# Kernel optimization log

Hardware: AMD Instinct MI355X
Metric: run time of the kernel (lower is better)

Reference implementation:

```python
import jax, jax.numpy as jnp
import numpy as np

N_NODES = 100000
N_EDGES = 1600000
D_FEAT = 128


def setup_inputs() -> dict:
    key = jax.random.key(0)
    k1, k2 = jax.random.split(key)
    x = jax.random.normal(k1, (N_NODES, D_FEAT), dtype=jnp.float32)
    edge_index = jax.random.randint(k2, (2, N_EDGES), 0, N_NODES, dtype=jnp.int64)
    return {"x": x, "edge_index": edge_index}


def reference(x, edge_index):
    # gather source/target node features: [E, D] each
    src = x[edge_index[0]]
    dst = x[edge_index[1]]
    # per-edge dot product -> [E], then sigmoid
    dot = jnp.sum(src * dst, axis=-1)
    return jax.nn.sigmoid(dot)
```

## Files before the change

kernel.cpp:

```cpp
#include <hip/hip_runtime.h>
#include <hip/hip_fp16.h>
#include <math.h>

#define D_FEAT 128

typedef _Float16 f16x2 __attribute__((ext_vector_type(2)));
struct alignas(16) h8v { f16x2 h[4]; };

__device__ __forceinline__ float dot8(const h8v& a, const h8v& b, float acc) {
#if __has_builtin(__builtin_amdgcn_fdot2)
#pragma unroll
    for (int k = 0; k < 4; ++k)
        acc = __builtin_amdgcn_fdot2(a.h[k], b.h[k], acc, false);
#else
#pragma unroll
    for (int k = 0; k < 4; ++k) {
        acc += (float)a.h[k].x * (float)b.h[k].x;
        acc += (float)a.h[k].y * (float)b.h[k].y;
    }
#endif
    return acc;
}

__device__ __forceinline__ float sigmoid_fast(float x) {
    return 1.0f / (1.0f + __builtin_exp2f(-1.44269504f * x));
}

__global__ __launch_bounds__(256) void convert_x_fp16_kernel(
    const float* __restrict__ x, __half* __restrict__ xh, int n_elems)
{
    int i = blockIdx.x * blockDim.x + threadIdx.x;
    int base = i * 8;
    if (base >= n_elems) return;
    const float4* p = reinterpret_cast<const float4*>(x + base);
    float4 f0 = p[0];
    float4 f1 = p[1];
    __half2 h[4];
    h[0] = __floats2half2_rn(f0.x, f0.y);
    h[1] = __floats2half2_rn(f0.z, f0.w);
    h[2] = __floats2half2_rn(f1.x, f1.y);
    h[3] = __floats2half2_rn(f1.z, f1.w);
    *reinterpret_cast<float4*>(xh + base) = *reinterpret_cast<float4*>(h);
}

__global__ __launch_bounds__(256) void edge_dot_sigmoid_fp16_kernel(
    const __half* __restrict__ xh,
    const int* __restrict__ ei,
    float* __restrict__ out,
    int n_edges)
{
    const int lane = threadIdx.x & 15;
    const int grp  = threadIdx.x >> 4;
    const int base = blockIdx.x * 32;
    const int e0 = base + grp;
    const int e1 = base + 16 + grp;

    if (e0 >= n_edges) return;

    const int s0 = ei[e0];
    const int d0 = ei[n_edges + e0];
    const bool has1 = (e1 < n_edges);
    const int s1 = has1 ? ei[e1] : s0;
    const int d1 = has1 ? ei[n_edges + e1] : d0;

    const h8v* __restrict__ xrow = reinterpret_cast<const h8v*>(xh);

    h8v a0 = xrow[(size_t)s0 * 16 + lane];
    h8v b0 = xrow[(size_t)d0 * 16 + lane];
    h8v a1 = xrow[(size_t)s1 * 16 + lane];
    h8v b1 = xrow[(size_t)d1 * 16 + lane];

    float acc0 = dot8(a0, b0, 0.f);
    float acc1 = dot8(a1, b1, 0.f);

    acc0 += __shfl_xor(acc0, 1, 16);
    acc0 += __shfl_xor(acc0, 2, 16);
    acc0 += __shfl_xor(acc0, 4, 16);
    acc0 += __shfl_xor(acc0, 8, 16);

    acc1 += __shfl_xor(acc1, 1, 16);
    acc1 += __shfl_xor(acc1, 2, 16);
    acc1 += __shfl_xor(acc1, 4, 16);
    acc1 += __shfl_xor(acc1, 8, 16);

    if (lane == 0) {
        out[e0] = sigmoid_fast(acc0);
        if (has1) out[e1] = sigmoid_fast(acc1);
    }
}

__global__ __launch_bounds__(256) void edge_dot_sigmoid_fp32_kernel(
    const float* __restrict__ x,
    const int* __restrict__ ei,
    float* __restrict__ out,
    int n_edges)
{
    const int lane = threadIdx.x & 15;
    const int e = blockIdx.x * 16 + (threadIdx.x >> 4);
    if (e >= n_edges) return;

    const int s = ei[e];
    const int d = ei[n_edges + e];

    const float4* sp = reinterpret_cast<const float4*>(x + (size_t)s * D_FEAT) + lane * 2;
    const float4* dp = reinterpret_cast<const float4*>(x + (size_t)d * D_FEAT) + lane * 2;

    float4 a0 = sp[0], a1 = sp[1], b0 = dp[0], b1 = dp[1];

    float acc = a0.x * b0.x + a0.y * b0.y + a0.z * b0.z + a0.w * b0.w
              + a1.x * b1.x + a1.y * b1.y + a1.z * b1.z + a1.w * b1.w;

    acc += __shfl_xor(acc, 1, 16);
    acc += __shfl_xor(acc, 2, 16);
    acc += __shfl_xor(acc, 4, 16);
    acc += __shfl_xor(acc, 8, 16);

    if (lane == 0) out[e] = sigmoid_fast(acc);
}

extern "C" void kernel_launch(void* const* d_in, const int* in_sizes, int n_in,
                              void* d_out, int out_size, void* d_ws, size_t ws_size,
                              hipStream_t stream) {
    const float* x   = (const float*)d_in[0];
    const int*   ei  = (const int*)d_in[1];
    float*       out = (float*)d_out;

    const int n_x     = in_sizes[0];
    const int n_edges = in_sizes[1] / 2;

    const size_t need = (size_t)n_x * sizeof(__half);
    if (ws_size >= need) {
        __half* xh = (__half*)d_ws;
        int n_chunks = (n_x + 7) / 8;
        convert_x_fp16_kernel<<<(n_chunks + 255) / 256, 256, 0, stream>>>(x, xh, n_x);
        dim3 grid((n_edges + 31) / 32);
        edge_dot_sigmoid_fp16_kernel<<<grid, 256, 0, stream>>>(xh, ei, out, n_edges);
    } else {
        dim3 grid((n_edges + 15) / 16);
        edge_dot_sigmoid_fp32_kernel<<<grid, 256, 0, stream>>>(x, ei, out, n_edges);
    }
}
```

Before: 111.5 us.

## Bucket edges by source node and swizzle workgroups across XCDs for cache locality

Adds a histogram, scan and scatter pipeline that bins edges by source node range into 1024 buckets. The dot kernel then walks the sorted edges, with workgroup ids remapped so each XCD handles a contiguous range, aiming for source row reuse in each XCD's L2. The cost is several extra kernel launches, atomics, extra index traffic (ss/sd/se arrays), and scattered output writes through the permutation.

```diff
diff --git a/kernel.cpp b/kernel.cpp
--- a/kernel.cpp
+++ b/kernel.cpp
@@ -3,6 +3,8 @@
 #include <math.h>
 
 #define D_FEAT 128
+#define NB 1024
+#define SCH 16384
 
 typedef _Float16 f16x2 __attribute__((ext_vector_type(2)));
 struct alignas(16) h8v { f16x2 h[4]; };
@@ -43,6 +45,122 @@
     *reinterpret_cast<float4*>(xh + base) = *reinterpret_cast<float4*>(h);
 }
 
+__global__ __launch_bounds__(256) void hist_kernel(
+    const int* __restrict__ ei, int n_edges, int shift, int* __restrict__ hist)
+{
+    __shared__ int h[NB];
+    for (int i = threadIdx.x; i < NB; i += 256) h[i] = 0;
+    __syncthreads();
+    for (int e = blockIdx.x * 256 + threadIdx.x; e < n_edges; e += gridDim.x * 256)
+        atomicAdd(&h[ei[e] >> shift], 1);
+    __syncthreads();
+    for (int i = threadIdx.x; i < NB; i += 256) {
+        int c = h[i];
+        if (c) atomicAdd(&hist[i], c);
+    }
+}
+
+__global__ __launch_bounds__(1024) void scan_kernel(
+    const int* __restrict__ hist, int* __restrict__ cursor)
+{
+    __shared__ int tmp[NB];
+    int t = threadIdx.x;
+    int own = hist[t];
+    tmp[t] = own;
+    __syncthreads();
+    for (int off = 1; off < NB; off <<= 1) {
+        int v = (t >= off) ? tmp[t - off] : 0;
+        __syncthreads();
+        tmp[t] += v;
+        __syncthreads();
+    }
+    cursor[t] = tmp[t] - own;
+}
+
+__global__ __launch_bounds__(256) void scatter_kernel(
+    const int* __restrict__ ei, int n_edges, int shift, int* __restrict__ cursor,
+    int* __restrict__ ss, int* __restrict__ sd, int* __restrict__ se)
+{
+    __shared__ int h[NB];
+    __shared__ int gbase[NB];
+    const int t = threadIdx.x;
+    for (int i = t; i < NB; i += 256) h[i] = 0;
+    __syncthreads();
+    const int c0 = blockIdx.x * SCH;
+    const int cend = min(n_edges, c0 + SCH);
+    for (int e = c0 + t; e < cend; e += 256)
+        atomicAdd(&h[ei[e] >> shift], 1);
+    __syncthreads();
+    for (int i = t; i < NB; i += 256) {
+        int c = h[i];
+        gbase[i] = c ? atomicAdd(&cursor[i], c) : 0;
+        h[i] = 0;
+    }
+    __syncthreads();
+    for (int e = c0 + t; e < cend; e += 256) {
+        int s = ei[e];
+        int b = s >> shift;
+        int loc = atomicAdd(&h[b], 1);
+        int pos = gbase[b] + loc;
+        ss[pos] = s;
+        sd[pos] = ei[n_edges + e];
+        se[pos] = e;
+    }
+}
+
+__global__ __launch_bounds__(256) void edge_dot_sigmoid_sorted_kernel(
+    const __half* __restrict__ xh,
+    const int* __restrict__ ss,
+    const int* __restrict__ sd,
+    const int* __restrict__ se,
+    float* __restrict__ out,
+    int n_edges, int q, int r)
+{
+    const int bid = blockIdx.x;
+    const int xcd = bid & 7;
+    const int idx = bid >> 3;
+    const int swz = (xcd < r) ? (xcd * (q + 1) + idx)
+                              : (r * (q + 1) + (xcd - r) * q + idx);
+
+    const int lane = threadIdx.x & 15;
+    const int grp  = threadIdx.x >> 4;
+    const int base = swz * 32;
+    const int e0 = base + grp;
+    const int e1 = base + 16 + grp;
+    if (e0 >= n_edges) return;
+
+    const int s0 = ss[e0];
+    const int d0 = sd[e0];
+    const bool has1 = (e1 < n_edges);
+    const int s1 = has1 ? ss[e1] : s0;
+    const int d1 = has1 ? sd[e1] : d0;
+
+    const h8v* __restrict__ xrow = reinterpret_cast<const h8v*>(xh);
+
+    h8v a0 = xrow[(size_t)s0 * 16 + lane];
+    h8v b0 = xrow[(size_t)d0 * 16 + lane];
+    h8v a1 = xrow[(size_t)s1 * 16 + lane];
+    h8v b1 = xrow[(size_t)d1 * 16 + lane];
+
+    float acc0 = dot8(a0, b0, 0.f);
+    float acc1 = dot8(a1, b1, 0.f);
+
+    acc0 += __shfl_xor(acc0, 1, 16);
+    acc0 += __shfl_xor(acc0, 2, 16);
+    acc0 += __shfl_xor(acc0, 4, 16);
+    acc0 += __shfl_xor(acc0, 8, 16);
+
+    acc1 += __shfl_xor(acc1, 1, 16);
+    acc1 += __shfl_xor(acc1, 2, 16);
+    acc1 += __shfl_xor(acc1, 4, 16);
+    acc1 += __shfl_xor(acc1, 8, 16);
+
+    if (lane == 0) {
+        out[se[e0]] = sigmoid_fast(acc0);
+        if (has1) out[se[e1]] = sigmoid_fast(acc1);
+    }
+}
+
 __global__ __launch_bounds__(256) void edge_dot_sigmoid_fp16_kernel(
     const __half* __restrict__ xh,
     const int* __restrict__ ei,
@@ -54,7 +172,6 @@
     const int base = blockIdx.x * 32;
     const int e0 = base + grp;
     const int e1 = base + 16 + grp;
-
     if (e0 >= n_edges) return;
 
     const int s0 = ei[e0];
@@ -127,9 +244,42 @@
 
     const int n_x     = in_sizes[0];
     const int n_edges = in_sizes[1] / 2;
-
-    const size_t need = (size_t)n_x * sizeof(__half);
-    if (ws_size >= need) {
+    const int n_nodes = n_x / D_FEAT;
+
+    size_t off_xh = 0;
+    size_t off_ss = ((size_t)n_x * 2 + 255) & ~(size_t)255;
+    size_t off_sd = off_ss + (size_t)n_edges * 4;
+    size_t off_se = off_sd + (size_t)n_edges * 4;
+    size_t off_hist = off_se + (size_t)n_edges * 4;
+    size_t off_cur  = off_hist + NB * 4;
+    size_t need_full = off_cur + NB * 4;
+    size_t need_fp16 = (size_t)n_x * 2;
+
+    if (ws_size >= need_full) {
+        __half* xh  = (__half*)((char*)d_ws + off_xh);
+        int* ss     = (int*)((char*)d_ws + off_ss);
+        int* sd     = (int*)((char*)d_ws + off_sd);
+        int* se     = (int*)((char*)d_ws + off_se);
+        int* hist   = (int*)((char*)d_ws + off_hist);
+        int* cursor = (int*)((char*)d_ws + off_cur);
+
+        int shift = 0;
+        while (((n_nodes - 1) >> shift) >= NB) shift++;
+
+        int n_chunks = (n_x + 7) / 8;
+        convert_x_fp16_kernel<<<(n_chunks + 255) / 256, 256, 0, stream>>>(x, xh, n_x);
+
+        hipMemsetAsync(hist, 0, NB * 4, stream);
+        hist_kernel<<<2048, 256, 0, stream>>>(ei, n_edges, shift, hist);
+        scan_kernel<<<1, 1024, 0, stream>>>(hist, cursor);
+        scatter_kernel<<<(n_edges + SCH - 1) / SCH, 256, 0, stream>>>(
+            ei, n_edges, shift, cursor, ss, sd, se);
+
+        int nwg = (n_edges + 31) / 32;
+        int q = nwg / 8, r = nwg % 8;
+        edge_dot_sigmoid_sorted_kernel<<<nwg, 256, 0, stream>>>(
+            xh, ss, sd, se, out, n_edges, q, r);
+    } else if (ws_size >= need_fp16) {
         __half* xh = (__half*)d_ws;
         int n_chunks = (n_x + 7) / 8;
         convert_x_fp16_kernel<<<(n_chunks + 255) / 256, 256, 0, stream>>>(x, xh, n_x);
```

After: 208.5 us. 87.0% more time.
